# Optimization experiments

Hardware: AMD Instinct MI355X
Metric: run time of the kernel (lower is better)

The kernel has to match this reference:

```python
import jax, jax.numpy as jnp
import numpy as np

H1, H2, F1, F2 = 16, 16, 8, 1

def gcn_conv(x, src, dst, W, b, n_nodes):
    # PyG GCNConv: add self-loops (done by caller), deg-normalized mean-style aggregation
    h = x @ W  # [N, out]
    deg = jax.ops.segment_sum(jnp.ones_like(dst, dtype=h.dtype), dst, num_segments=n_nodes)
    dinv = jnp.where(deg > 0, deg ** -0.5, 0.0)
    norm = dinv[src] * dinv[dst]  # [E]
    agg = jax.ops.segment_sum(h[src] * norm[:, None], dst, num_segments=n_nodes)
    return agg + b


def setup_inputs() -> dict:
    key = jax.random.key(0)
    ks = jax.random.split(key, 12)
    N, E, G, NG = 320000, 5120000, 1000, 32
    x = jax.random.normal(ks[0], (N, 1), dtype=jnp.float32)
    edge_index = jax.random.randint(ks[1], (2, E), 0, N, dtype=jnp.int64)
    y = jax.random.normal(ks[2], (NG * G,), dtype=jnp.float32)
    gene_idx = jax.random.randint(ks[3], (1, G), 0, N // NG, dtype=jnp.int64)
    s = lambda fi, fo: (2.0 / (fi + fo)) ** 0.5
    return {
        'x': x, 'edge_index': edge_index, 'y': y, 'gene_idx': gene_idx, 'num_graphs': NG,
        'W1': jax.random.normal(ks[4], (1, H1), dtype=jnp.float32) * s(1, H1),
        'b1': jnp.zeros((H1,), dtype=jnp.float32),
        'W2': jax.random.normal(ks[5], (H1, H2), dtype=jnp.float32) * s(H1, H2),
        'b2': jnp.zeros((H2,), dtype=jnp.float32),
        'fc1_W': jax.random.normal(ks[6], (H2, F1), dtype=jnp.float32) * s(H2, F1),
        'fc1_b': jnp.zeros((F1,), dtype=jnp.float32),
        'fc2_W': jax.random.normal(ks[7], (F1, F2), dtype=jnp.float32) * s(F1, F2),
        'fc2_b': jnp.zeros((F2,), dtype=jnp.float32),
    }


def reference(x, edge_index, y, gene_idx, num_graphs, W1, b1, W2, b2, fc1_W, fc1_b, fc2_W, fc2_b):
    N = x.shape[0]
    loops = jnp.arange(N, dtype=edge_index.dtype)
    src = jnp.concatenate([edge_index[0], loops])
    dst = jnp.concatenate([edge_index[1], loops])

    h = jax.nn.relu(gcn_conv(x, src, dst, W1, b1, N))
    # F.dropout(p=0.4) is a no-op for a deterministic reference (identity at eval)
    h = jax.nn.relu(gcn_conv(h, src, dst, W2, b2, N))

    # vectorized form of the python gather loop: idx + i * nodes_per_graph, i = 0..reps-1
    nodes_per_graph = N // num_graphs
    reps = y.shape[0] // gene_idx.shape[1]
    offsets = (jnp.arange(reps, dtype=gene_idx.dtype) * nodes_per_graph)[:, None]
    all_idx = (gene_idx[0][None, :] + offsets).reshape(-1)  # [reps*G]
    t = h[all_idx]  # [reps*G, 16]

    t = jax.nn.relu(t @ fc1_W + fc1_b)
    return t @ fc2_W + fc2_b
```

## Files before the change

### kernel.cpp

```cpp
#include <hip/hip_runtime.h>


#define MAXB 17
#define RS_BITS 10
#define RS (1 << RS_BITS)
#define SRC_BITS 19
#define SRC_MASK ((1u << SRC_BITS) - 1u)
#define CMAX 160
#define PSTRIDE (CMAX * 8)
#define BK_BT 512
#define BK_EPT 16
#define BK_TILE (BK_BT * BK_EPT)

__global__ void k_fill_f(float* __restrict__ w, float v, int n) {
    int i = blockIdx.x * blockDim.x + threadIdx.x;
    if (i < n) w[i] = v;
}
__global__ void k_fill_i(int* __restrict__ w, int v, int n) {
    int i = blockIdx.x * blockDim.x + threadIdx.x;
    if (i < n) w[i] = v;
}

__global__ void k_prep(const float* __restrict__ W1, const float* __restrict__ b1,
                       float* __restrict__ bnd, int* __restrict__ prepI) {
    if (threadIdx.x != 0 || blockIdx.x != 0) return;
    float t[16]; int type[16]; int pos[16];
    float thr[16]; int nt = 0;
    for (int j = 0; j < 16; j++) {
        float W = W1[j], B = b1[j];
        if (W > 0.f)      { type[j] = 0; t[j] = -B / W; }
        else if (W < 0.f) { type[j] = 1; t[j] = -B / W; }
        else              { type[j] = (B > 0.f) ? 2 : 3; t[j] = 0.f; }
    }
    for (int j = 0; j < 16; j++) {
        if (type[j] > 1) continue;
        float v = t[j];
        int k = 0; while (k < nt && thr[k] < v) k++;
        if (!(k < nt && thr[k] == v)) {
            for (int m = nt; m > k; m--) thr[m] = thr[m - 1];
            thr[k] = v; nt++;
        }
    }
    int K = nt + 1;
    for (int j = 0; j < 16; j++) {
        if (type[j] <= 1) { int k = 0; while (thr[k] != t[j]) k++; pos[j] = k; }
        else pos[j] = 0;
    }
    for (int k = 0; k < 16; k++) bnd[k] = (k < nt) ? thr[k] : 3.4e38f;
    prepI[0] = K;
    for (int k = 0; k < K; k++) {
        unsigned m = 0;
        for (int j = 0; j < 16; j++) {
            bool act;
            if (type[j] == 0)      act = (k >= pos[j] + 1);
            else if (type[j] == 1) act = (k <= pos[j]);
            else                   act = (type[j] == 2);
            if (act) m |= (1u << j);
        }
        prepI[1 + k] = (int)m;
    }
}

__global__ void k_mark(const int* __restrict__ gene_idx, int* __restrict__ slot,
                       int G, int M, int npg, int N) {
    int i = blockIdx.x * blockDim.x + threadIdx.x;
    if (i >= M) return;
    int node = gene_idx[i % G] + (i / G) * npg;
    if ((unsigned)node < (unsigned)N) slot[node] = i;
}

__global__ void k_cmap(int* __restrict__ cm, int* __restrict__ cslot, int* __restrict__ mc,
                       int N, int R) {
    __shared__ int cnt;
    int r = blockIdx.x;
    if (r >= R) return;
    if (threadIdx.x == 0) cnt = 0;
    __syncthreads();
    int b0 = r << RS_BITS;
    for (int i = threadIdx.x; i < RS; i += blockDim.x) {
        int v = b0 + i;
        if (v >= N) continue;
        int sl = cm[v];
        int out;
        if (sl >= 0) {
            int c = atomicAdd(&cnt, 1);
            if (c < CMAX) { cslot[r * CMAX + c] = sl; out = c; }
            else out = -(sl + 2);
        } else out = -1;
        cm[v] = out;
    }
    __syncthreads();
    if (threadIdx.x == 0) mc[r] = min(cnt, CMAX);
}


__global__ void k_hist(const int* __restrict__ dst, int* __restrict__ histG,
                       int E, int N, int R) {
    __shared__ int h[512];
    for (int i = threadIdx.x; i < R; i += blockDim.x) h[i] = 0;
    __syncthreads();
    int E4 = E >> 2;
    const int4* d4 = (const int4*)dst;
    for (int e = blockIdx.x * blockDim.x + threadIdx.x; e < E4; e += gridDim.x * blockDim.x) {
        int4 d = d4[e];
        if ((unsigned)d.x < (unsigned)N) atomicAdd(&h[d.x >> RS_BITS], 1);
        if ((unsigned)d.y < (unsigned)N) atomicAdd(&h[d.y >> RS_BITS], 1);
        if ((unsigned)d.z < (unsigned)N) atomicAdd(&h[d.z >> RS_BITS], 1);
        if ((unsigned)d.w < (unsigned)N) atomicAdd(&h[d.w >> RS_BITS], 1);
    }
    for (int e = (E4 << 2) + blockIdx.x * blockDim.x + threadIdx.x; e < E;
         e += gridDim.x * blockDim.x) {
        int d = dst[e];
        if ((unsigned)d < (unsigned)N) atomicAdd(&h[d >> RS_BITS], 1);
    }
    __syncthreads();
    for (int i = threadIdx.x; i < R; i += blockDim.x) {
        int c = h[i];
        if (c) atomicAdd(&histG[i], c);
    }
}

__global__ void k_scan(const int* __restrict__ histG, int* __restrict__ base,
                       int* __restrict__ cursor, int R) {
    __shared__ int a[512];
    int t = threadIdx.x;
    int v = (t < R) ? ((histG[t] + 3) & ~3) : 0;
    a[t] = v;
    __syncthreads();
    for (int off = 1; off < 512; off <<= 1) {
        int add = (t >= off) ? a[t - off] : 0;
        __syncthreads();
        a[t] += add;
        __syncthreads();
    }
    if (t < R) { int ex = a[t] - v; base[t] = ex; cursor[t] = ex; }
}

__global__ void __launch_bounds__(BK_BT)
k_bucket(const int* __restrict__ src, const int* __restrict__ dst,
         int* __restrict__ cursorG, unsigned* __restrict__ bucket,
         int E, int N, int R, int cap) {
    __shared__ int cnt[512];
    __shared__ int baseL[512];
    int tile0 = blockIdx.x * BK_TILE;
    for (int i = threadIdx.x; i < R; i += BK_BT) cnt[i] = 0;
    __syncthreads();
    int ds[BK_EPT], ss[BK_EPT];
#pragma unroll
    for (int c = 0; c < 4; c++) {
        int e0 = tile0 + c * (BK_BT * 4) + threadIdx.x * 4;
#pragma unroll
        for (int k = 0; k < 4; k++) {
            int e = e0 + k;
            int idx = c * 4 + k;
            ds[idx] = -1;
            if (e < E) {
                int d = dst[e], s = src[e];
                if ((unsigned)d < (unsigned)N && (unsigned)s < (unsigned)N) {
                    ds[idx] = d; ss[idx] = s;
                    atomicAdd(&cnt[d >> RS_BITS], 1);
                }
            }
        }
    }
    __syncthreads();
    for (int r = threadIdx.x; r < R; r += BK_BT) {
        int c = cnt[r];
        baseL[r] = c > 0 ? atomicAdd(&cursorG[r], c) : 0;
        cnt[r] = 0;
    }
    __syncthreads();
#pragma unroll
    for (int i = 0; i < BK_EPT; i++) {
        int d = ds[i];
        if (d < 0) continue;
        int r = d >> RS_BITS;
        int o = atomicAdd(&cnt[r], 1);
        int idx = baseL[r] + o;
        if ((unsigned)idx < (unsigned)cap)
            bucket[idx] = ((unsigned)(d & (RS - 1)) << SRC_BITS) | (unsigned)ss[i];
    }
}


__global__ void __launch_bounds__(1024)
k_degR2(const unsigned* __restrict__ bucket, const int* __restrict__ base,
        const int* __restrict__ histG, int* __restrict__ pDeg, int cap, int S) {
    __shared__ int degL[RS];
    int r = blockIdx.x / S, q = blockIdx.x % S;
    int nb = base[r];
    int cnt = min(histG[r], cap - nb);
    if (cnt < 0) cnt = 0;
    int lo = (int)(((long long)cnt * q / S) & ~3LL);
    int hi = (q == S - 1) ? cnt : (int)(((long long)cnt * (q + 1) / S) & ~3LL);
    for (int i = threadIdx.x; i < RS; i += blockDim.x) degL[i] = 0;
    __syncthreads();
    for (int i = lo + threadIdx.x * 4; i < hi; i += blockDim.x * 4) {
        uint4 e4 = *(const uint4*)(bucket + nb + i);
        if (i + 0 < hi) atomicAdd(&degL[e4.x >> SRC_BITS], 1);
        if (i + 1 < hi) atomicAdd(&degL[e4.y >> SRC_BITS], 1);
        if (i + 2 < hi) atomicAdd(&degL[e4.z >> SRC_BITS], 1);
        if (i + 3 < hi) atomicAdd(&degL[e4.w >> SRC_BITS], 1);
    }
    __syncthreads();
    int* out = pDeg + (size_t)(r * S + q) * RS;
    for (int i = threadIdx.x; i < RS; i += blockDim.x) out[i] = degL[i];
}

__global__ void k_dinvp2(const int* __restrict__ pDeg, const float* __restrict__ x,
                         float* __restrict__ sd, float* __restrict__ p, int N, int S) {
    int v = blockIdx.x * blockDim.x + threadIdx.x;
    if (v >= N) return;
    int r = v >> RS_BITS, l = v & (RS - 1);
    int deg = 0;
    for (int q = 0; q < S; q++) deg += pDeg[(size_t)(r * S + q) * RS + l];
    float di = rsqrtf((float)deg + 1.0f);
    sd[2 * v + 1] = di;
    p[v] = x[v] * di;
}

__global__ void __launch_bounds__(1024)
k_t1R2(const unsigned* __restrict__ bucket, const int* __restrict__ base,
       const int* __restrict__ histG, const float* __restrict__ p,
       float* __restrict__ pT1, int cap, int S) {
    __shared__ float accL[RS];
    int r = blockIdx.x / S, q = blockIdx.x % S;
    int nb = base[r];
    int cnt = min(histG[r], cap - nb);
    if (cnt < 0) cnt = 0;
    int lo = (int)(((long long)cnt * q / S) & ~3LL);
    int hi = (q == S - 1) ? cnt : (int)(((long long)cnt * (q + 1) / S) & ~3LL);
    for (int i = threadIdx.x; i < RS; i += blockDim.x) accL[i] = 0.f;
    __syncthreads();
    for (int i = lo + threadIdx.x * 4; i < hi; i += blockDim.x * 4) {
        uint4 e4 = *(const uint4*)(bucket + nb + i);
        if (i + 0 < hi) atomicAdd(&accL[e4.x >> SRC_BITS], p[e4.x & SRC_MASK]);
        if (i + 1 < hi) atomicAdd(&accL[e4.y >> SRC_BITS], p[e4.y & SRC_MASK]);
        if (i + 2 < hi) atomicAdd(&accL[e4.z >> SRC_BITS], p[e4.z & SRC_MASK]);
        if (i + 3 < hi) atomicAdd(&accL[e4.w >> SRC_BITS], p[e4.w & SRC_MASK]);
    }
    __syncthreads();
    float* out = pT1 + (size_t)(r * S + q) * RS;
    for (int i = threadIdx.x; i < RS; i += blockDim.x) out[i] = accL[i];
}

__global__ void k_s3(const float* __restrict__ pT1, const float* __restrict__ p,
                     float* __restrict__ sd, int N, int S) {
    int v = blockIdx.x * blockDim.x + threadIdx.x;
    if (v >= N) return;
    int r = v >> RS_BITS, l = v & (RS - 1);
    float t1 = 0.f;
    for (int q = 0; q < S; q++) t1 += pT1[(size_t)(r * S + q) * RS + l];
    sd[2 * v] = sd[2 * v + 1] * (t1 + p[v]);
}

__global__ void __launch_bounds__(1024)
k_aggS(const unsigned* __restrict__ bucket, const int* __restrict__ base,
       const int* __restrict__ histG, const float* __restrict__ sd,
       const int* __restrict__ cm, const float* __restrict__ bnd,
       const int* __restrict__ prepI, float* __restrict__ pAgg,
       float* __restrict__ aggb8, int N, int cap, int S) {
    __shared__ float acc[PSTRIDE];
    __shared__ int cmapL[RS];
    __shared__ float sB[3];
    __shared__ int sK;
    if (threadIdx.x == 0) sK = prepI[0];
    if (threadIdx.x < 3) sB[threadIdx.x] = bnd[threadIdx.x];
    __syncthreads();
    int K = sK;
    if (K > 4) return;
    int r = blockIdx.x / S, q = blockIdx.x % S;
    int b0 = r << RS_BITS;
    for (int i = threadIdx.x; i < RS; i += blockDim.x) {
        int v = b0 + i;
        cmapL[i] = (v < N) ? cm[v] : -1;
    }
    for (int i = threadIdx.x; i < PSTRIDE; i += blockDim.x) acc[i] = 0.f;
    __syncthreads();
    int nb = base[r];
    int cnt = min(histG[r], cap - nb);
    if (cnt < 0) cnt = 0;
    int lo = (int)(((long long)cnt * q / S) & ~3LL);
    int hi = (q == S - 1) ? cnt : (int)(((long long)cnt * (q + 1) / S) & ~3LL);
    const float2* sd2 = (const float2*)sd;
    for (int i = lo + threadIdx.x * 4; i < hi; i += blockDim.x * 4) {
        uint4 e4 = *(const uint4*)(bucket + nb + i);
        unsigned ee[4] = {e4.x, e4.y, e4.z, e4.w};
#pragma unroll
        for (int k4 = 0; k4 < 4; k4++) {
            if (i + k4 >= hi) break;
            unsigned e = ee[k4];
            int c = cmapL[e >> SRC_BITS];
            if (c == -1) continue;
            float2 v = sd2[e & SRC_MASK];
            int b = 0;
            for (int k = 0; k < K - 1; k++) b += (v.x > sB[k]) ? 1 : 0;
            if (c >= 0) {
                atomicAdd(&acc[c * 8 + 2 * b], v.x * v.y);
                atomicAdd(&acc[c * 8 + 2 * b + 1], v.y);
            } else {
                int sl = -(c + 2);
                atomicAdd(&aggb8[(size_t)sl * 8 + 2 * b], v.x * v.y);
                atomicAdd(&aggb8[(size_t)sl * 8 + 2 * b + 1], v.y);
            }
        }
    }
    __syncthreads();
    float* out = pAgg + (size_t)(r * S + q) * PSTRIDE;
    for (int i = threadIdx.x; i < PSTRIDE; i += blockDim.x) out[i] = acc[i];
}

__global__ void k_aggMerge(const float* __restrict__ pAgg, const int* __restrict__ cslot,
                           const int* __restrict__ mc, float* __restrict__ aggb8,
                           int R, int S) {
    int idx = blockIdx.x * blockDim.x + threadIdx.x;
    int per = CMAX * 8;
    int r = idx / per;
    if (r >= R) return;
    int rem = idx % per;
    int c = rem >> 3, j = rem & 7;
    if (c >= mc[r]) return;
    int sl = cslot[r * CMAX + c];
    if (sl < 0) return;
    float sum = 0.f;
    for (int q = 0; q < S; q++) sum += pAgg[(size_t)(r * S + q) * PSTRIDE + c * 8 + j];
    aggb8[(size_t)sl * 8 + j] = sum;
}

__global__ void k_fillWide(const int* __restrict__ prepI, float* __restrict__ wide, int n) {
    if (prepI[0] <= 4) return;
    int i = blockIdx.x * blockDim.x + threadIdx.x;
    if (i < n) wide[i] = 0.f;
}


__global__ void k_deg(const int* __restrict__ dst, float* __restrict__ deg, int E, int N) {
    int e = blockIdx.x * blockDim.x + threadIdx.x;
    if (e >= E) return;
    int d = dst[e];
    if ((unsigned)d < (unsigned)N) atomicAdd(&deg[d], 1.0f);
}

__global__ void k_dinv_p(const float* __restrict__ x, float* __restrict__ degv,
                         float* __restrict__ p, int N) {
    int v = blockIdx.x * blockDim.x + threadIdx.x;
    if (v < N) {
        float di = rsqrtf(degv[v] + 1.0f);
        degv[v] = di;
        p[v] = x[v] * di;
    }
}

__global__ void k_scatter1(const int* __restrict__ src, const int* __restrict__ dst,
                           const float* __restrict__ p, float* __restrict__ t1, int E, int N) {
    int e = blockIdx.x * blockDim.x + threadIdx.x;
    if (e >= E) return;
    int s = src[e];
    int d = dst[e];
    if ((unsigned)s < (unsigned)N && (unsigned)d < (unsigned)N)
        atomicAdd(&t1[d], p[s]);
}

__global__ void k_s(const float* __restrict__ p, const float* __restrict__ dinv,
                    float* __restrict__ t1, int N) {
    int v = blockIdx.x * blockDim.x + threadIdx.x;
    if (v < N) t1[v] = dinv[v] * (t1[v] + p[v]);
}

__global__ void k_agg_atomic(const int* __restrict__ src, const int* __restrict__ dst,
                             const float* __restrict__ sA, const float* __restrict__ dA,
                             int str, const int* __restrict__ cm, const int* __restrict__ cslot,
                             const float* __restrict__ bnd, const int* __restrict__ prepI,
                             float* __restrict__ wide, int E, int N, int force, int mode) {
    __shared__ float sB[16];
    __shared__ int sK;
    if (threadIdx.x == 0) sK = prepI[0];
    if (threadIdx.x < 16) sB[threadIdx.x] = bnd[threadIdx.x];
    __syncthreads();
    int K = sK;
    if (!force && K <= 4) return;
    int T = K - 1;
    for (int e = blockIdx.x * blockDim.x + threadIdx.x; e < E; e += gridDim.x * blockDim.x) {
        int d = dst[e];
        if ((unsigned)d >= (unsigned)N) continue;
        int c = cm[d];
        int sl;
        if (mode == 0) sl = c;
        else sl = (c >= 0) ? cslot[(d >> RS_BITS) * CMAX + c] : (c <= -2 ? -(c + 2) : -1);
        if (sl < 0) continue;
        int sv = src[e];
        if ((unsigned)sv >= (unsigned)N) continue;
        float sval = sA[(size_t)sv * str];
        float di = dA[(size_t)sv * str];
        int b = 0;
        for (int i = 0; i < T; i++) b += (sval > sB[i]) ? 1 : 0;
        float* row = wide + (size_t)sl * (2 * MAXB) + 2 * b;
        atomicAdd(row, sval * di);
        atomicAdd(row + 1, di);
    }
}

__global__ void k_final(const float* __restrict__ aggb8, const float* __restrict__ wide,
                        const float* __restrict__ sA, const float* __restrict__ dA, int str,
                        const int* __restrict__ gene_idx, const int* __restrict__ cm,
                        const int* __restrict__ cslot, const int* __restrict__ prepI,
                        const float* __restrict__ W1, const float* __restrict__ b1,
                        const float* __restrict__ W2, const float* __restrict__ b2,
                        const float* __restrict__ f1W, const float* __restrict__ f1b,
                        const float* __restrict__ f2W, const float* __restrict__ f2b,
                        float* __restrict__ out, int G, int M, int npg, int N, int mode) {
    __shared__ float sW1[16], sb1[16], sW2[256], sb2[16], sf1[128], sf1b[8], sf2[8], sf2b[1];
    __shared__ int sMask[MAXB], sK;
    for (int i = threadIdx.x; i < 256; i += blockDim.x) sW2[i] = W2[i];
    for (int i = threadIdx.x; i < 128; i += blockDim.x) sf1[i] = f1W[i];
    if (threadIdx.x < 16) { sW1[threadIdx.x] = W1[threadIdx.x]; sb1[threadIdx.x] = b1[threadIdx.x]; sb2[threadIdx.x] = b2[threadIdx.x]; }
    if (threadIdx.x < 8)  { sf1b[threadIdx.x] = f1b[threadIdx.x]; sf2[threadIdx.x] = f2W[threadIdx.x]; }
    if (threadIdx.x == 0) { sf2b[0] = f2b[0]; sK = prepI[0]; }
    if (threadIdx.x < MAXB) sMask[threadIdx.x] = prepI[1 + threadIdx.x];
    __syncthreads();

    int i = blockIdx.x * blockDim.x + threadIdx.x;
    if (i >= M) return;
    int node = gene_idx[i % G] + (i / G) * npg;
    if ((unsigned)node >= (unsigned)N) { out[i] = 0.0f; return; }
    int K = sK;
    int c = cm[node];
    int sl;
    if (mode == 0) sl = c;
    else sl = (c >= 0) ? cslot[(node >> RS_BITS) * CMAX + c] : (c <= -2 ? -(c + 2) : -1);

    float di = dA[(size_t)node * str];
    float sval = sA[(size_t)node * str];

    float bu[MAXB], bw[MAXB];
    if (sl >= 0) {
        const float* row = (mode == 1 && K <= 4) ? (aggb8 + (size_t)sl * 8)
                                                 : (wide + (size_t)sl * (2 * MAXB));
        for (int k = 0; k < K; k++) { bu[k] = row[2 * k]; bw[k] = row[2 * k + 1]; }
    } else {
        for (int k = 0; k < K; k++) { bu[k] = 0.f; bw[k] = 0.f; }
    }

    float a[16];
#pragma unroll
    for (int j = 0; j < 16; j++) {
        float Su = 0.f, Sw = 0.f;
        for (int k = 0; k < K; k++) {
            if ((sMask[k] >> j) & 1) { Su += bu[k]; Sw += bw[k]; }
        }
        float aggj = sW1[j] * Su + sb1[j] * Sw;
        float qself = fmaxf(fmaf(sW1[j], sval, sb1[j]), 0.0f) * di;
        a[j] = di * (aggj + qself);
    }
    float h2[16];
#pragma unroll
    for (int j = 0; j < 16; j++) {
        float acc = sb2[j];
#pragma unroll
        for (int k = 0; k < 16; k++) acc = fmaf(a[k], sW2[k * 16 + j], acc);
        h2[j] = fmaxf(acc, 0.0f);
    }
    float f1[8];
#pragma unroll
    for (int j = 0; j < 8; j++) {
        float acc = sf1b[j];
#pragma unroll
        for (int k = 0; k < 16; k++) acc = fmaf(h2[k], sf1[k * 8 + j], acc);
        f1[j] = fmaxf(acc, 0.0f);
    }
    float o = sf2b[0];
#pragma unroll
    for (int k = 0; k < 8; k++) o = fmaf(f1[k], sf2[k], o);
    out[i] = o;
}

extern "C" void kernel_launch(void* const* d_in, const int* in_sizes, int n_in,
                              void* d_out, int out_size, void* d_ws, size_t ws_size,
                              hipStream_t stream) {
    const float* x        = (const float*)d_in[0];
    const int*   ei       = (const int*)d_in[1];
    const int*   gene_idx = (const int*)d_in[3];
    const float* W1  = (const float*)d_in[5];
    const float* b1  = (const float*)d_in[6];
    const float* W2  = (const float*)d_in[7];
    const float* b2  = (const float*)d_in[8];
    const float* f1W = (const float*)d_in[9];
    const float* f1b = (const float*)d_in[10];
    const float* f2W = (const float*)d_in[11];
    const float* f2b = (const float*)d_in[12];
    float* out = (float*)d_out;

    int N = in_sizes[0];
    int E = in_sizes[1] / 2;
    int M = in_sizes[2];
    int G = in_sizes[3];
    int npg = (int)(((long long)N * (long long)G) / (long long)M);

    const int* src = ei;
    const int* dst = ei + E;

    int R = (N + RS - 1) >> RS_BITS;
    int cap = E + 4 * R + 4;
    const int tb = 256;

    float* ws = (float*)d_ws;
    size_t off = 0;
    float*    sd     = ws + off;              off += (size_t)2 * N;
    int*      cm     = (int*)(ws + off);      off += (size_t)N;
    float*    p      = ws + off;              off += (size_t)N;
    float*    aggb8  = ws + off;              off += (size_t)8 * M;
    unsigned* bucket = (unsigned*)(ws + off); off += (size_t)cap;
    float*    wide   = (float*)bucket;
    int*      cslot  = (int*)(ws + off);      off += (size_t)R * CMAX;
    int*      mc     = (int*)(ws + off);      off += (size_t)R;
    int*      histG  = (int*)(ws + off);      off += (size_t)R;
    int*      baseA  = (int*)(ws + off);      off += (size_t)R;
    int*      cursor = (int*)(ws + off);      off += (size_t)R;
    float*    bnd    = ws + off;              off += 16;
    int*      prepI  = (int*)(ws + off);      off += 20;
    size_t base_need = off;

    int S = 4;
    while (S > 1 && (base_need + (size_t)R * S * PSTRIDE) * 4 > ws_size) S >>= 1;
    float* partial = ws + base_need;
    int*   partialI = (int*)partial;
    size_t need = (base_need + (size_t)R * S * PSTRIDE) * 4;

    bool use_new = (need <= ws_size) && (N < (1 << SRC_BITS)) && (R <= 512) &&
                   ((size_t)cap * 4 >= (size_t)2 * MAXB * M * 4);

    if (use_new) {
        int BTr = (S == 1) ? 1024 : 256;
        k_fill_i<<<(N + tb - 1) / tb, tb, 0, stream>>>(cm, -1, N);
        k_fill_i<<<(R + tb - 1) / tb, tb, 0, stream>>>(histG, 0, R);
        k_prep<<<1, 64, 0, stream>>>(W1, b1, bnd, prepI);
        k_mark<<<(M + tb - 1) / tb, tb, 0, stream>>>(gene_idx, cm, G, M, npg, N);
        k_cmap<<<R, tb, 0, stream>>>(cm, cslot, mc, N, R);
        k_hist<<<512, tb, 0, stream>>>(dst, histG, E, N, R);
        k_scan<<<1, 512, 0, stream>>>(histG, baseA, cursor, R);
        int ntiles = (E + BK_TILE - 1) / BK_TILE;
        k_bucket<<<ntiles, BK_BT, 0, stream>>>(src, dst, cursor, bucket, E, N, R, cap);
        k_degR2<<<R * S, BTr, 0, stream>>>(bucket, baseA, histG, partialI, cap, S);
        k_dinvp2<<<(N + tb - 1) / tb, tb, 0, stream>>>(partialI, x, sd, p, N, S);
        k_t1R2<<<R * S, BTr, 0, stream>>>(bucket, baseA, histG, p, partial, cap, S);
        k_s3<<<(N + tb - 1) / tb, tb, 0, stream>>>(partial, p, sd, N, S);
        k_fill_f<<<(8 * M + tb - 1) / tb, tb, 0, stream>>>(aggb8, 0.0f, 8 * M);
        k_aggS<<<R * S, BTr, 0, stream>>>(bucket, baseA, histG, sd, cm, bnd, prepI,
                                          partial, aggb8, N, cap, S);
        k_aggMerge<<<(R * CMAX * 8 + tb - 1) / tb, tb, 0, stream>>>(partial, cslot, mc,
                                                                    aggb8, R, S);
        int wn = 2 * MAXB * M;
        k_fillWide<<<(wn + tb - 1) / tb, tb, 0, stream>>>(prepI, wide, wn);
        k_agg_atomic<<<2048, tb, 0, stream>>>(src, dst, sd, sd + 1, 2, cm, cslot, bnd,
                                              prepI, wide, E, N, 0, 1);
        k_final<<<(M + tb - 1) / tb, tb, 0, stream>>>(aggb8, wide, sd, sd + 1, 2, gene_idx,
                                                      cm, cslot, prepI, W1, b1, W2, b2,
                                                      f1W, f1b, f2W, f2b, out, G, M, npg, N,
                                                      1);
    } else {
        float* deg   = ws;
        float* t1o   = ws + (size_t)N;
        float* pO    = ws + 2 * (size_t)N;
        int*   slotO = (int*)(ws + 3 * (size_t)N);
        float* wideO = ws + 4 * (size_t)N;
        float* bndO  = wideO + (size_t)2 * MAXB * M;
        int*   prepO = (int*)(bndO + 16);

        k_fill_f<<<(2 * N + tb - 1) / tb, tb, 0, stream>>>(deg, 0.0f, 2 * N);
        k_fill_i<<<(N + tb - 1) / tb, tb, 0, stream>>>(slotO, -1, N);
        k_fill_f<<<(2 * MAXB * M + tb - 1) / tb, tb, 0, stream>>>(wideO, 0.0f, 2 * MAXB * M);
        k_prep<<<1, 64, 0, stream>>>(W1, b1, bndO, prepO);
        k_mark<<<(M + tb - 1) / tb, tb, 0, stream>>>(gene_idx, slotO, G, M, npg, N);
        k_deg<<<(E + tb - 1) / tb, tb, 0, stream>>>(dst, deg, E, N);
        k_dinv_p<<<(N + tb - 1) / tb, tb, 0, stream>>>(x, deg, pO, N);
        k_scatter1<<<(E + tb - 1) / tb, tb, 0, stream>>>(src, dst, pO, t1o, E, N);
        k_s<<<(N + tb - 1) / tb, tb, 0, stream>>>(pO, deg, t1o, N);
        k_agg_atomic<<<2048, tb, 0, stream>>>(src, dst, t1o, deg, 1, slotO, (int*)0, bndO,
                                              prepO, wideO, E, N, 1, 0);
        k_final<<<(M + tb - 1) / tb, tb, 0, stream>>>((float*)0, wideO, t1o, deg, 1, gene_idx,
                                                      slotO, (int*)0, prepO, W1, b1, W2, b2,
                                                      f1W, f1b, f2W, f2b, out, G, M, npg, N,
                                                      0);
    }
}
```

Measured before the change: 262.8 us.

## Split buckets into marked/unmarked regions so aggS scans only marked edges

The bucketing pass now classifies each edge by whether its destination is a gathered output node, using a gene bitmap. Marked edges are written from the front of each region and unmarked ones from the back, with sentinel padding. The layer-2 aggregation kernel then scans only the marked prefix in one block per region and writes results directly, which removes the split partials and the separate merge kernel. The cost is a second set of atomics and a bitmap lookup in bucketing, a fill of the bucket buffer with sentinels, and sentinel checks in the degree and t1 passes.

```diff
diff --git a/kernel.cpp b/kernel.cpp
--- a/kernel.cpp
+++ b/kernel.cpp
@@ -6,8 +6,9 @@
 #define RS (1 << RS_BITS)
 #define SRC_BITS 19
 #define SRC_MASK ((1u << SRC_BITS) - 1u)
+#define SENT 0xFFFFFFFFu
 #define CMAX 160
-#define PSTRIDE (CMAX * 8)
+#define NPGW_MAX 2048
 #define BK_BT 512
 #define BK_EPT 16
 #define BK_TILE (BK_BT * BK_EPT)
@@ -21,20 +22,34 @@
     if (i < n) w[i] = v;
 }
 
-__global__ void k_prep(const float* __restrict__ W1, const float* __restrict__ b1,
-                       float* __restrict__ bnd, int* __restrict__ prepI) {
-    if (threadIdx.x != 0 || blockIdx.x != 0) return;
-    float t[16]; int type[16]; int pos[16];
+__global__ void k_gprep(const float* __restrict__ W1, const float* __restrict__ b1,
+                        const int* __restrict__ gene_idx,
+                        float* __restrict__ bnd, int* __restrict__ prepI,
+                        int* __restrict__ gmap, unsigned* __restrict__ gbit,
+                        int G, int npg, int npgw) {
+    int t = threadIdx.x;
+    for (int i = t; i < npg; i += 256) gmap[i] = -1;
+    for (int i = t; i < npgw; i += 256) gbit[i] = 0;
+    __syncthreads();
+    for (int g = t; g < G; g += 256) {
+        int gi = gene_idx[g];
+        if ((unsigned)gi < (unsigned)npg) {
+            gmap[gi] = g;
+            atomicOr(&gbit[gi >> 5], 1u << (gi & 31));
+        }
+    }
+    if (t != 0) return;
+    float tt[16]; int type[16]; int pos[16];
     float thr[16]; int nt = 0;
     for (int j = 0; j < 16; j++) {
         float W = W1[j], B = b1[j];
-        if (W > 0.f)      { type[j] = 0; t[j] = -B / W; }
-        else if (W < 0.f) { type[j] = 1; t[j] = -B / W; }
-        else              { type[j] = (B > 0.f) ? 2 : 3; t[j] = 0.f; }
+        if (W > 0.f)      { type[j] = 0; tt[j] = -B / W; }
+        else if (W < 0.f) { type[j] = 1; tt[j] = -B / W; }
+        else              { type[j] = (B > 0.f) ? 2 : 3; tt[j] = 0.f; }
     }
     for (int j = 0; j < 16; j++) {
         if (type[j] > 1) continue;
-        float v = t[j];
+        float v = tt[j];
         int k = 0; while (k < nt && thr[k] < v) k++;
         if (!(k < nt && thr[k] == v)) {
             for (int m = nt; m > k; m--) thr[m] = thr[m - 1];
@@ -43,7 +58,7 @@
     }
     int K = nt + 1;
     for (int j = 0; j < 16; j++) {
-        if (type[j] <= 1) { int k = 0; while (thr[k] != t[j]) k++; pos[j] = k; }
+        if (type[j] <= 1) { int k = 0; while (thr[k] != tt[j]) k++; pos[j] = k; }
         else pos[j] = 0;
     }
     for (int k = 0; k < 16; k++) bnd[k] = (k < nt) ? thr[k] : 3.4e38f;
@@ -61,32 +76,30 @@
     }
 }
 
-__global__ void k_mark(const int* __restrict__ gene_idx, int* __restrict__ slot,
-                       int G, int M, int npg, int N) {
-    int i = blockIdx.x * blockDim.x + threadIdx.x;
-    if (i >= M) return;
-    int node = gene_idx[i % G] + (i / G) * npg;
-    if ((unsigned)node < (unsigned)N) slot[node] = i;
-}
-
-__global__ void k_cmap(int* __restrict__ cm, int* __restrict__ cslot, int* __restrict__ mc,
-                       int N, int R) {
+__global__ void k_cmap(const int* __restrict__ gmap, const unsigned* __restrict__ gbit,
+                       int* __restrict__ cm, int* __restrict__ cslot, int* __restrict__ mc,
+                       int N, int R, int npg, int reps, int G) {
     __shared__ int cnt;
     int r = blockIdx.x;
     if (r >= R) return;
     if (threadIdx.x == 0) cnt = 0;
     __syncthreads();
     int b0 = r << RS_BITS;
-    for (int i = threadIdx.x; i < RS; i += blockDim.x) {
+    for (int i = threadIdx.x; i < RS; i += 256) {
         int v = b0 + i;
         if (v >= N) continue;
-        int sl = cm[v];
-        int out;
-        if (sl >= 0) {
-            int c = atomicAdd(&cnt, 1);
-            if (c < CMAX) { cslot[r * CMAX + c] = sl; out = c; }
-            else out = -(sl + 2);
-        } else out = -1;
+        int rep = v / npg;
+        int gi = v - rep * npg;
+        int out = -1;
+        if (rep < reps && ((gbit[gi >> 5] >> (gi & 31)) & 1u)) {
+            int g = gmap[gi];
+            if (g >= 0) {
+                int sl = rep * G + g;
+                int c = atomicAdd(&cnt, 1);
+                if (c < CMAX) { cslot[r * CMAX + c] = sl; out = c; }
+                else out = -(sl + 2);
+            }
+        }
         cm[v] = out;
     }
     __syncthreads();
@@ -121,7 +134,7 @@
 }
 
 __global__ void k_scan(const int* __restrict__ histG, int* __restrict__ base,
-                       int* __restrict__ cursor, int R) {
+                       int* __restrict__ mcur, int* __restrict__ ucur, int R) {
     __shared__ int a[512];
     int t = threadIdx.x;
     int v = (t < R) ? ((histG[t] + 3) & ~3) : 0;
@@ -133,19 +146,21 @@
         a[t] += add;
         __syncthreads();
     }
-    if (t < R) { int ex = a[t] - v; base[t] = ex; cursor[t] = ex; }
+    if (t < R) { int ex = a[t] - v; base[t] = ex; mcur[t] = ex; ucur[t] = ex + v; }
 }
 
 __global__ void __launch_bounds__(BK_BT)
 k_bucket(const int* __restrict__ src, const int* __restrict__ dst,
-         int* __restrict__ cursorG, unsigned* __restrict__ bucket,
-         int E, int N, int R, int cap) {
-    __shared__ int cnt[512];
-    __shared__ int baseL[512];
+         const unsigned* __restrict__ gbit,
+         int* __restrict__ mcurG, int* __restrict__ ucurG, unsigned* __restrict__ bucket,
+         int E, int N, int R, int cap, int npg, int reps, int npgw) {
+    __shared__ unsigned bitL[NPGW_MAX];
+    __shared__ int mcnt[512], ucnt[512], mbase[512], ubase[512];
     int tile0 = blockIdx.x * BK_TILE;
-    for (int i = threadIdx.x; i < R; i += BK_BT) cnt[i] = 0;
-    __syncthreads();
-    int ds[BK_EPT], ss[BK_EPT];
+    for (int i = threadIdx.x; i < npgw; i += BK_BT) bitL[i] = gbit[i];
+    for (int i = threadIdx.x; i < R; i += BK_BT) { mcnt[i] = 0; ucnt[i] = 0; }
+    __syncthreads();
+    int ds[BK_EPT]; unsigned ss[BK_EPT];
 #pragma unroll
     for (int c = 0; c < 4; c++) {
         int e0 = tile0 + c * (BK_BT * 4) + threadIdx.x * 4;
@@ -157,17 +172,24 @@
             if (e < E) {
                 int d = dst[e], s = src[e];
                 if ((unsigned)d < (unsigned)N && (unsigned)s < (unsigned)N) {
-                    ds[idx] = d; ss[idx] = s;
-                    atomicAdd(&cnt[d >> RS_BITS], 1);
+                    int rep = d / npg;
+                    int gi = d - rep * npg;
+                    unsigned m = (rep < reps && ((bitL[gi >> 5] >> (gi & 31)) & 1u)) ? 1u : 0u;
+                    ds[idx] = d;
+                    ss[idx] = (unsigned)s | (m << 30);
+                    atomicAdd(m ? &mcnt[d >> RS_BITS] : &ucnt[d >> RS_BITS], 1);
                 }
             }
         }
     }
     __syncthreads();
     for (int r = threadIdx.x; r < R; r += BK_BT) {
-        int c = cnt[r];
-        baseL[r] = c > 0 ? atomicAdd(&cursorG[r], c) : 0;
-        cnt[r] = 0;
+        int c = mcnt[r];
+        mbase[r] = c > 0 ? atomicAdd(&mcurG[r], c) : 0;
+        mcnt[r] = 0;
+        int u = ucnt[r];
+        ubase[r] = u > 0 ? (atomicSub(&ucurG[r], u) - u) : 0;
+        ucnt[r] = 0;
     }
     __syncthreads();
 #pragma unroll
@@ -175,10 +197,11 @@
         int d = ds[i];
         if (d < 0) continue;
         int r = d >> RS_BITS;
-        int o = atomicAdd(&cnt[r], 1);
-        int idx = baseL[r] + o;
+        unsigned m = ss[i] >> 30;
+        int o = atomicAdd(m ? &mcnt[r] : &ucnt[r], 1);
+        int idx = (m ? mbase[r] : ubase[r]) + o;
         if ((unsigned)idx < (unsigned)cap)
-            bucket[idx] = ((unsigned)(d & (RS - 1)) << SRC_BITS) | (unsigned)ss[i];
+            bucket[idx] = ((unsigned)(d & (RS - 1)) << SRC_BITS) | (ss[i] & SRC_MASK);
     }
 }
 
@@ -189,7 +212,7 @@
     __shared__ int degL[RS];
     int r = blockIdx.x / S, q = blockIdx.x % S;
     int nb = base[r];
-    int cnt = min(histG[r], cap - nb);
+    int cnt = min((histG[r] + 3) & ~3, cap - nb);
     if (cnt < 0) cnt = 0;
     int lo = (int)(((long long)cnt * q / S) & ~3LL);
     int hi = (q == S - 1) ? cnt : (int)(((long long)cnt * (q + 1) / S) & ~3LL);
@@ -197,10 +220,10 @@
     __syncthreads();
     for (int i = lo + threadIdx.x * 4; i < hi; i += blockDim.x * 4) {
         uint4 e4 = *(const uint4*)(bucket + nb + i);
-        if (i + 0 < hi) atomicAdd(&degL[e4.x >> SRC_BITS], 1);
-        if (i + 1 < hi) atomicAdd(&degL[e4.y >> SRC_BITS], 1);
-        if (i + 2 < hi) atomicAdd(&degL[e4.z >> SRC_BITS], 1);
-        if (i + 3 < hi) atomicAdd(&degL[e4.w >> SRC_BITS], 1);
+        if (i + 0 < hi && e4.x != SENT) atomicAdd(&degL[e4.x >> SRC_BITS], 1);
+        if (i + 1 < hi && e4.y != SENT) atomicAdd(&degL[e4.y >> SRC_BITS], 1);
+        if (i + 2 < hi && e4.z != SENT) atomicAdd(&degL[e4.z >> SRC_BITS], 1);
+        if (i + 3 < hi && e4.w != SENT) atomicAdd(&degL[e4.w >> SRC_BITS], 1);
     }
     __syncthreads();
     int* out = pDeg + (size_t)(r * S + q) * RS;
@@ -226,7 +249,7 @@
     __shared__ float accL[RS];
     int r = blockIdx.x / S, q = blockIdx.x % S;
     int nb = base[r];
-    int cnt = min(histG[r], cap - nb);
+    int cnt = min((histG[r] + 3) & ~3, cap - nb);
     if (cnt < 0) cnt = 0;
     int lo = (int)(((long long)cnt * q / S) & ~3LL);
     int hi = (q == S - 1) ? cnt : (int)(((long long)cnt * (q + 1) / S) & ~3LL);
@@ -234,10 +257,10 @@
     __syncthreads();
     for (int i = lo + threadIdx.x * 4; i < hi; i += blockDim.x * 4) {
         uint4 e4 = *(const uint4*)(bucket + nb + i);
-        if (i + 0 < hi) atomicAdd(&accL[e4.x >> SRC_BITS], p[e4.x & SRC_MASK]);
-        if (i + 1 < hi) atomicAdd(&accL[e4.y >> SRC_BITS], p[e4.y & SRC_MASK]);
-        if (i + 2 < hi) atomicAdd(&accL[e4.z >> SRC_BITS], p[e4.z & SRC_MASK]);
-        if (i + 3 < hi) atomicAdd(&accL[e4.w >> SRC_BITS], p[e4.w & SRC_MASK]);
+        if (i + 0 < hi && e4.x != SENT) atomicAdd(&accL[e4.x >> SRC_BITS], p[e4.x & SRC_MASK]);
+        if (i + 1 < hi && e4.y != SENT) atomicAdd(&accL[e4.y >> SRC_BITS], p[e4.y & SRC_MASK]);
+        if (i + 2 < hi && e4.z != SENT) atomicAdd(&accL[e4.z >> SRC_BITS], p[e4.z & SRC_MASK]);
+        if (i + 3 < hi && e4.w != SENT) atomicAdd(&accL[e4.w >> SRC_BITS], p[e4.w & SRC_MASK]);
     }
     __syncthreads();
     float* out = pT1 + (size_t)(r * S + q) * RS;
@@ -254,13 +277,13 @@
     sd[2 * v] = sd[2 * v + 1] * (t1 + p[v]);
 }
 
-__global__ void __launch_bounds__(1024)
-k_aggS(const unsigned* __restrict__ bucket, const int* __restrict__ base,
-       const int* __restrict__ histG, const float* __restrict__ sd,
-       const int* __restrict__ cm, const float* __restrict__ bnd,
-       const int* __restrict__ prepI, float* __restrict__ pAgg,
-       float* __restrict__ aggb8, int N, int cap, int S) {
-    __shared__ float acc[PSTRIDE];
+__global__ void k_aggS(const unsigned* __restrict__ bucket, const int* __restrict__ base,
+                       const int* __restrict__ mcur, const int* __restrict__ histG,
+                       const float* __restrict__ sd, const int* __restrict__ cm,
+                       const int* __restrict__ cslot, const int* __restrict__ mc,
+                       const float* __restrict__ bnd, const int* __restrict__ prepI,
+                       float* __restrict__ aggb8, int N, int cap) {
+    __shared__ float acc[CMAX * 8];
     __shared__ int cmapL[RS];
     __shared__ float sB[3];
     __shared__ int sK;
@@ -269,26 +292,27 @@
     __syncthreads();
     int K = sK;
     if (K > 4) return;
-    int r = blockIdx.x / S, q = blockIdx.x % S;
+    int r = blockIdx.x;
     int b0 = r << RS_BITS;
-    for (int i = threadIdx.x; i < RS; i += blockDim.x) {
+    for (int i = threadIdx.x; i < RS; i += 256) {
         int v = b0 + i;
         cmapL[i] = (v < N) ? cm[v] : -1;
     }
-    for (int i = threadIdx.x; i < PSTRIDE; i += blockDim.x) acc[i] = 0.f;
+    for (int i = threadIdx.x; i < CMAX * 8; i += 256) acc[i] = 0.f;
     __syncthreads();
     int nb = base[r];
-    int cnt = min(histG[r], cap - nb);
-    if (cnt < 0) cnt = 0;
-    int lo = (int)(((long long)cnt * q / S) & ~3LL);
-    int hi = (q == S - 1) ? cnt : (int)(((long long)cnt * (q + 1) / S) & ~3LL);
+    int pad = min((histG[r] + 3) & ~3, cap - nb);
+    if (pad < 0) pad = 0;
+    int mlen = mcur[r] - nb;
+    if (mlen < 0) mlen = 0;
+    if (mlen > pad) mlen = pad;
     const float2* sd2 = (const float2*)sd;
-    for (int i = lo + threadIdx.x * 4; i < hi; i += blockDim.x * 4) {
+    for (int i = threadIdx.x * 4; i < mlen; i += 256 * 4) {
         uint4 e4 = *(const uint4*)(bucket + nb + i);
         unsigned ee[4] = {e4.x, e4.y, e4.z, e4.w};
 #pragma unroll
         for (int k4 = 0; k4 < 4; k4++) {
-            if (i + k4 >= hi) break;
+            if (i + k4 >= mlen) break;
             unsigned e = ee[k4];
             int c = cmapL[e >> SRC_BITS];
             if (c == -1) continue;
@@ -306,25 +330,12 @@
         }
     }
     __syncthreads();
-    float* out = pAgg + (size_t)(r * S + q) * PSTRIDE;
-    for (int i = threadIdx.x; i < PSTRIDE; i += blockDim.x) out[i] = acc[i];
-}
-
-__global__ void k_aggMerge(const float* __restrict__ pAgg, const int* __restrict__ cslot,
-                           const int* __restrict__ mc, float* __restrict__ aggb8,
-                           int R, int S) {
-    int idx = blockIdx.x * blockDim.x + threadIdx.x;
-    int per = CMAX * 8;
-    int r = idx / per;
-    if (r >= R) return;
-    int rem = idx % per;
-    int c = rem >> 3, j = rem & 7;
-    if (c >= mc[r]) return;
-    int sl = cslot[r * CMAX + c];
-    if (sl < 0) return;
-    float sum = 0.f;
-    for (int q = 0; q < S; q++) sum += pAgg[(size_t)(r * S + q) * PSTRIDE + c * 8 + j];
-    aggb8[(size_t)sl * 8 + j] = sum;
+    int mcR = mc[r];
+    for (int idx = threadIdx.x; idx < mcR * 8; idx += 256) {
+        int c = idx >> 3, j = idx & 7;
+        int sl = cslot[r * CMAX + c];
+        if (sl >= 0) aggb8[(size_t)sl * 8 + j] = acc[idx];
+    }
 }
 
 __global__ void k_fillWide(const int* __restrict__ prepI, float* __restrict__ wide, int n) {
@@ -333,6 +344,14 @@
     if (i < n) wide[i] = 0.f;
 }
 
+
+__global__ void k_mark(const int* __restrict__ gene_idx, int* __restrict__ slot,
+                       int G, int M, int npg, int N) {
+    int i = blockIdx.x * blockDim.x + threadIdx.x;
+    if (i >= M) return;
+    int node = gene_idx[i % G] + (i / G) * npg;
+    if ((unsigned)node < (unsigned)N) slot[node] = i;
+}
 
 __global__ void k_deg(const int* __restrict__ dst, float* __restrict__ deg, int E, int N) {
     int e = blockIdx.x * blockDim.x + threadIdx.x;
@@ -495,6 +514,8 @@
     int M = in_sizes[2];
     int G = in_sizes[3];
     int npg = (int)(((long long)N * (long long)G) / (long long)M);
+    int reps = (G > 0) ? M / G : 0;
+    int npgw = (npg + 31) / 32;
 
     const int* src = ei;
     const int* dst = ei + E;
@@ -511,44 +532,46 @@
     float*    aggb8  = ws + off;              off += (size_t)8 * M;
     unsigned* bucket = (unsigned*)(ws + off); off += (size_t)cap;
     float*    wide   = (float*)bucket;
+    int*      gmap   = (int*)(ws + off);      off += (size_t)npg;
+    unsigned* gbit   = (unsigned*)(ws + off); off += (size_t)npgw;
     int*      cslot  = (int*)(ws + off);      off += (size_t)R * CMAX;
     int*      mc     = (int*)(ws + off);      off += (size_t)R;
     int*      histG  = (int*)(ws + off);      off += (size_t)R;
     int*      baseA  = (int*)(ws + off);      off += (size_t)R;
-    int*      cursor = (int*)(ws + off);      off += (size_t)R;
+    int*      mcur   = (int*)(ws + off);      off += (size_t)R;
+    int*      ucur   = (int*)(ws + off);      off += (size_t)R;
     float*    bnd    = ws + off;              off += 16;
     int*      prepI  = (int*)(ws + off);      off += 20;
     size_t base_need = off;
 
     int S = 4;
-    while (S > 1 && (base_need + (size_t)R * S * PSTRIDE) * 4 > ws_size) S >>= 1;
+    while (S > 1 && (base_need + (size_t)R * S * RS) * 4 > ws_size) S >>= 1;
     float* partial = ws + base_need;
     int*   partialI = (int*)partial;
-    size_t need = (base_need + (size_t)R * S * PSTRIDE) * 4;
+    size_t need = (base_need + (size_t)R * S * RS) * 4;
 
     bool use_new = (need <= ws_size) && (N < (1 << SRC_BITS)) && (R <= 512) &&
+                   (npg >= 1) && (npg <= NPGW_MAX * 32) && (reps >= 1) &&
                    ((size_t)cap * 4 >= (size_t)2 * MAXB * M * 4);
 
     if (use_new) {
         int BTr = (S == 1) ? 1024 : 256;
-        k_fill_i<<<(N + tb - 1) / tb, tb, 0, stream>>>(cm, -1, N);
+        k_fill_i<<<(cap + tb - 1) / tb, tb, 0, stream>>>((int*)bucket, -1, cap);
         k_fill_i<<<(R + tb - 1) / tb, tb, 0, stream>>>(histG, 0, R);
-        k_prep<<<1, 64, 0, stream>>>(W1, b1, bnd, prepI);
-        k_mark<<<(M + tb - 1) / tb, tb, 0, stream>>>(gene_idx, cm, G, M, npg, N);
-        k_cmap<<<R, tb, 0, stream>>>(cm, cslot, mc, N, R);
+        k_gprep<<<1, 256, 0, stream>>>(W1, b1, gene_idx, bnd, prepI, gmap, gbit, G, npg, npgw);
+        k_cmap<<<R, tb, 0, stream>>>(gmap, gbit, cm, cslot, mc, N, R, npg, reps, G);
         k_hist<<<512, tb, 0, stream>>>(dst, histG, E, N, R);
-        k_scan<<<1, 512, 0, stream>>>(histG, baseA, cursor, R);
+        k_scan<<<1, 512, 0, stream>>>(histG, baseA, mcur, ucur, R);
         int ntiles = (E + BK_TILE - 1) / BK_TILE;
-        k_bucket<<<ntiles, BK_BT, 0, stream>>>(src, dst, cursor, bucket, E, N, R, cap);
+        k_bucket<<<ntiles, BK_BT, 0, stream>>>(src, dst, gbit, mcur, ucur, bucket,
+                                               E, N, R, cap, npg, reps, npgw);
         k_degR2<<<R * S, BTr, 0, stream>>>(bucket, baseA, histG, partialI, cap, S);
         k_dinvp2<<<(N + tb - 1) / tb, tb, 0, stream>>>(partialI, x, sd, p, N, S);
         k_t1R2<<<R * S, BTr, 0, stream>>>(bucket, baseA, histG, p, partial, cap, S);
         k_s3<<<(N + tb - 1) / tb, tb, 0, stream>>>(partial, p, sd, N, S);
         k_fill_f<<<(8 * M + tb - 1) / tb, tb, 0, stream>>>(aggb8, 0.0f, 8 * M);
-        k_aggS<<<R * S, BTr, 0, stream>>>(bucket, baseA, histG, sd, cm, bnd, prepI,
-                                          partial, aggb8, N, cap, S);
-        k_aggMerge<<<(R * CMAX * 8 + tb - 1) / tb, tb, 0, stream>>>(partial, cslot, mc,
-                                                                    aggb8, R, S);
+        k_aggS<<<R, tb, 0, stream>>>(bucket, baseA, mcur, histG, sd, cm, cslot, mc,
+                                     bnd, prepI, aggb8, N, cap);
         int wn = 2 * MAXB * M;
         k_fillWide<<<(wn + tb - 1) / tb, tb, 0, stream>>>(prepI, wide, wn);
         k_agg_atomic<<<2048, tb, 0, stream>>>(src, dst, sd, sd + 1, 2, cm, cslot, bnd,
@@ -569,7 +592,8 @@
         k_fill_f<<<(2 * N + tb - 1) / tb, tb, 0, stream>>>(deg, 0.0f, 2 * N);
         k_fill_i<<<(N + tb - 1) / tb, tb, 0, stream>>>(slotO, -1, N);
         k_fill_f<<<(2 * MAXB * M + tb - 1) / tb, tb, 0, stream>>>(wideO, 0.0f, 2 * MAXB * M);
-        k_prep<<<1, 64, 0, stream>>>(W1, b1, bndO, prepO);
+        k_gprep<<<1, 256, 0, stream>>>(W1, b1, gene_idx, bndO, prepO,
+                                       (int*)wideO, (unsigned*)(wideO + npg), 0, 1, 1);
         k_mark<<<(M + tb - 1) / tb, tb, 0, stream>>>(gene_idx, slotO, G, M, npg, N);
         k_deg<<<(E + tb - 1) / tb, tb, 0, stream>>>(dst, deg, E, N);
         k_dinv_p<<<(N + tb - 1) / tb, tb, 0, stream>>>(x, deg, pO, N);
```

After: 267.6 us. No clear change (+1.8%).
